# Kernel tuning notes

Hardware: AMD Instinct MI355X
Metric: run time of the kernel (lower is better)

## Reference

```python
import jax, jax.numpy as jnp
import numpy as np

T = 1024  # output_length
H = 15    # GRU hidden size
I = 10    # seed size
O = 128   # output_size
B = 512   # batch

def setup_inputs() -> dict:
    key = jax.random.key(0)
    ks = jax.random.split(key, 8)
    s = 1.0 / np.sqrt(H)
    return {
        "feed": jax.random.normal(ks[0], (B, 1, I), dtype=jnp.float32),
        "h0":   jax.random.uniform(ks[1], (B, H), dtype=jnp.float32),
        "W_ih": jax.random.normal(ks[2], (3 * H, I), dtype=jnp.float32) * s,
        "W_hh": jax.random.normal(ks[3], (3 * H, H), dtype=jnp.float32) * s,
        "b_ih": jax.random.normal(ks[4], (3 * H,), dtype=jnp.float32) * s,
        "b_hh": jax.random.normal(ks[5], (3 * H,), dtype=jnp.float32) * s,
        "W_out": jax.random.normal(ks[6], (O, H), dtype=jnp.float32) * s,
        "b_out": jnp.zeros((O,), dtype=jnp.float32),
    }

def reference(feed, h0, W_ih, W_hh, b_ih, b_hh, W_out, b_out):
    # feed is repeated along time in the original, so the input-gate
    # projection is identical at every step: compute it once.
    x = feed[:, 0, :]                         # [B, I]
    gi = x @ W_ih.T + b_ih                    # [B, 3H]
    i_r, i_z, i_n = jnp.split(gi, 3, axis=-1)  # torch GRU gate order: r, z, n

    def step(h, _):
        gh = h @ W_hh.T + b_hh                # [B, 3H]
        h_r, h_z, h_n = jnp.split(gh, 3, axis=-1)
        r = jax.nn.sigmoid(i_r + h_r)
        z = jax.nn.sigmoid(i_z + h_z)
        n = jnp.tanh(i_n + r * h_n)
        h_new = (1.0 - z) * n + z * h
        return h_new, h_new

    _, hs = jax.lax.scan(step, h0, None, length=T)  # [T, B, H]
    # Linear + sigmoid; original returns output.transpose(0,1) -> [T, B, O],
    # which scan's time-major layout already gives us.
    out = jax.nn.sigmoid(jnp.einsum("tbh,oh->tbo", hs, W_out) + b_out)
    return out
```

## Files before the change

kernel.cpp:

```cpp
#include <hip/hip_runtime.h>
#include <cstdint>

#define Tt 1024
#define Hh 15
#define Ii 10
#define Oo 128
#define Bb 512

typedef float v4f __attribute__((ext_vector_type(4)));

__device__ __forceinline__ float sigmoidf_(float x) {
    return 1.0f / (1.0f + __expf(-x));
}
__device__ __forceinline__ float tanhf_(float x) {
    return 1.0f - 2.0f / (__expf(2.0f * x) + 1.0f);
}

#define ROT(x, j) __int_as_float(__builtin_amdgcn_update_dpp( \
    0, __float_as_int(x), 0x120 + (j), 0xF, 0xF, true))

__global__ __launch_bounds__(64, 1) void gru_recur(
    const float* __restrict__ feed, const float* __restrict__ h0,
    const float* __restrict__ W_ih, const float* __restrict__ W_hh,
    const float* __restrict__ b_ih, const float* __restrict__ b_hh,
    float* __restrict__ hs)
{
    const int lane = threadIdx.x;
    const int g = lane >> 4;
    const int u = lane & 15;
    const int uu = (u < Hh) ? u : 0;
    const int b = blockIdx.x * 4 + g;

    int pr = __builtin_amdgcn_update_dpp(0, lane & 15, 0x121, 0xF, 0xF, true);
    int p0 = __builtin_amdgcn_readfirstlane(pr);
    const int dir = (p0 == 1) ? 1 : 15;

    float Wr[16], Wz[16], Wn[16];
    #pragma unroll
    for (int j = 0; j < 16; ++j) {
        int k = (uu + dir * j) & 15;
        bool ok = (k < Hh);
        int kk = ok ? k : 0;
        Wr[j] = ok ? W_hh[(uu         ) * Hh + kk] : 0.0f;
        Wz[j] = ok ? W_hh[(uu +     Hh) * Hh + kk] : 0.0f;
        Wn[j] = ok ? W_hh[(uu + 2 * Hh) * Hh + kk] : 0.0f;
    }

    float cr = b_ih[uu]          + b_hh[uu];
    float cz = b_ih[uu + Hh]     + b_hh[uu + Hh];
    float cn = b_ih[uu + 2 * Hh];
    float bn = b_hh[uu + 2 * Hh];
    #pragma unroll
    for (int i = 0; i < Ii; ++i) {
        float x = feed[b * Ii + i];
        cr += x * W_ih[(uu         ) * Ii + i];
        cz += x * W_ih[(uu +     Hh) * Ii + i];
        cn += x * W_ih[(uu + 2 * Hh) * Ii + i];
    }

    float hcur = (u < Hh) ? h0[b * Hh + uu] : 0.0f;
    size_t off = (size_t)b * 16 + u;

    for (int t = 0; t < Tt; ++t) {
        float hr[16];
        hr[0]  = hcur;
        hr[1]  = ROT(hcur, 1);   hr[2]  = ROT(hcur, 2);
        hr[3]  = ROT(hcur, 3);   hr[4]  = ROT(hcur, 4);
        hr[5]  = ROT(hcur, 5);   hr[6]  = ROT(hcur, 6);
        hr[7]  = ROT(hcur, 7);   hr[8]  = ROT(hcur, 8);
        hr[9]  = ROT(hcur, 9);   hr[10] = ROT(hcur, 10);
        hr[11] = ROT(hcur, 11);  hr[12] = ROT(hcur, 12);
        hr[13] = ROT(hcur, 13);  hr[14] = ROT(hcur, 14);
        hr[15] = ROT(hcur, 15);

        float ar[4] = {cr, 0.f, 0.f, 0.f};
        float az[4] = {cz, 0.f, 0.f, 0.f};
        float an[4] = {bn, 0.f, 0.f, 0.f};
        #pragma unroll
        for (int j = 0; j < 16; ++j) {
            ar[j & 3] += Wr[j] * hr[j];
            az[j & 3] += Wz[j] * hr[j];
            an[j & 3] += Wn[j] * hr[j];
        }
        float r = sigmoidf_((ar[0] + ar[1]) + (ar[2] + ar[3]));
        float z = sigmoidf_((az[0] + az[1]) + (az[2] + az[3]));
        float dn = (an[0] + an[1]) + (an[2] + an[3]);
        float n = tanhf_(cn + r * dn);
        float hnew = n + z * (hcur - n);

        hs[off] = hnew;
        off += (size_t)Bb * 16;
        hcur = hnew;
    }
}

__device__ __forceinline__ v4f ntload4(const float* p) {
    return __builtin_nontemporal_load((const v4f*)p);
}

__global__ __launch_bounds__(256) void gru_proj(
    const float* __restrict__ hs, const float* __restrict__ W_out,
    const float* __restrict__ b_out, float* __restrict__ out)
{
    const int q  = threadIdx.x & 31;
    const int gg = threadIdx.x >> 5;
    const int o0 = q * 4;

    float w[4][Hh];
    float bo[4];
    #pragma unroll
    for (int j = 0; j < 4; ++j) {
        bo[j] = b_out[o0 + j];
        #pragma unroll
        for (int k = 0; k < Hh; ++k) w[j][k] = W_out[(o0 + j) * Hh + k];
    }

    const int P = Tt * Bb;
    const int stride = gridDim.x * 8;
    int p = blockIdx.x * 8 + gg;
    if (p >= P) return;

    const float* hp = hs + (size_t)p * 16;
    v4f A = ntload4(hp), B_ = ntload4(hp + 4), C = ntload4(hp + 8), D = ntload4(hp + 12);

    while (true) {
        int pn = p + stride;
        bool more = pn < P;
        const float* hpn = hs + (size_t)(more ? pn : p) * 16;
        v4f A2 = ntload4(hpn), B2 = ntload4(hpn + 4),
            C2 = ntload4(hpn + 8), D2 = ntload4(hpn + 12);

        float h[Hh] = {A.x, A.y, A.z, A.w, B_.x, B_.y, B_.z, B_.w,
                       C.x, C.y, C.z, C.w, D.x, D.y, D.z};
        float acc[4];
        #pragma unroll
        for (int j = 0; j < 4; ++j) {
            float s0 = bo[j], s1 = 0.f;
            #pragma unroll
            for (int k = 0; k < Hh; k += 2) s0 += h[k] * w[j][k];
            #pragma unroll
            for (int k = 1; k < Hh; k += 2) s1 += h[k] * w[j][k];
            acc[j] = sigmoidf_(s0 + s1);
        }
        v4f res = {acc[0], acc[1], acc[2], acc[3]};
        __builtin_nontemporal_store(res, (v4f*)(out + (size_t)p * (size_t)Oo + o0));

        if (!more) break;
        p = pn; A = A2; B_ = B2; C = C2; D = D2;
    }
}

extern "C" void kernel_launch(void* const* d_in, const int* in_sizes, int n_in,
                              void* d_out, int out_size, void* d_ws, size_t ws_size,
                              hipStream_t stream) {
    const float* feed  = (const float*)d_in[0];
    const float* h0    = (const float*)d_in[1];
    const float* W_ih  = (const float*)d_in[2];
    const float* W_hh  = (const float*)d_in[3];
    const float* b_ih  = (const float*)d_in[4];
    const float* b_hh  = (const float*)d_in[5];
    const float* W_out = (const float*)d_in[6];
    const float* b_out = (const float*)d_in[7];
    float* out = (float*)d_out;
    float* hs  = (float*)d_ws;

    gru_recur<<<Bb / 4, 64, 0, stream>>>(feed, h0, W_ih, W_hh, b_ih, b_hh, hs);
    gru_proj<<<2048, 256, 0, stream>>>(hs, W_out, b_out, out);
}
```

Baseline: 528.2 us.

## Fuse GRU recurrence and output projection into one per-batch kernel

Merges the recurrence and output projection into a single kernel with one wavefront per batch element. Each step broadcasts the hidden state with readlane and each lane computes two of the 128 outputs, storing them directly. This removes the hs workspace round trip and the second launch. In exchange, the 4x redundant recurrence lanes (16 lanes each replicated), 15 serial readlanes per step and projection work now sit on the sequential critical path, and the grid grows from 128 to 512 wavefronts.

```diff
diff --git a/kernel.cpp b/kernel.cpp
--- a/kernel.cpp
+++ b/kernel.cpp
@@ -7,7 +7,7 @@
 #define Oo 128
 #define Bb 512
 
-typedef float v4f __attribute__((ext_vector_type(4)));
+typedef float v2f __attribute__((ext_vector_type(2)));
 
 __device__ __forceinline__ float sigmoidf_(float x) {
     return 1.0f / (1.0f + __expf(-x));
@@ -19,21 +19,20 @@
 #define ROT(x, j) __int_as_float(__builtin_amdgcn_update_dpp( \
     0, __float_as_int(x), 0x120 + (j), 0xF, 0xF, true))
 
-__global__ __launch_bounds__(64, 1) void gru_recur(
+__global__ __launch_bounds__(64, 1) void gru_fused(
     const float* __restrict__ feed, const float* __restrict__ h0,
     const float* __restrict__ W_ih, const float* __restrict__ W_hh,
     const float* __restrict__ b_ih, const float* __restrict__ b_hh,
-    float* __restrict__ hs)
+    const float* __restrict__ W_out, const float* __restrict__ b_out,
+    float* __restrict__ out)
 {
     const int lane = threadIdx.x;
-    const int g = lane >> 4;
     const int u = lane & 15;
     const int uu = (u < Hh) ? u : 0;
-    const int b = blockIdx.x * 4 + g;
+    const int b = blockIdx.x;
 
     int pr = __builtin_amdgcn_update_dpp(0, lane & 15, 0x121, 0xF, 0xF, true);
-    int p0 = __builtin_amdgcn_readfirstlane(pr);
-    const int dir = (p0 == 1) ? 1 : 15;
+    const int dir = (__builtin_amdgcn_readfirstlane(pr) == 1) ? 1 : 15;
 
     float Wr[16], Wz[16], Wn[16];
     #pragma unroll
@@ -58,8 +57,17 @@
         cn += x * W_ih[(uu + 2 * Hh) * Ii + i];
     }
 
+    const int o0 = lane * 2;
+    float wp0[Hh], wp1[Hh];
+    #pragma unroll
+    for (int k = 0; k < Hh; ++k) {
+        wp0[k] = W_out[(o0    ) * Hh + k];
+        wp1[k] = W_out[(o0 + 1) * Hh + k];
+    }
+    const float bo0 = b_out[o0], bo1 = b_out[o0 + 1];
+
     float hcur = (u < Hh) ? h0[b * Hh + uu] : 0.0f;
-    size_t off = (size_t)b * 16 + u;
+    float* outp = out + (size_t)b * Oo + o0;
 
     for (int t = 0; t < Tt; ++t) {
         float hr[16];
@@ -88,65 +96,28 @@
         float n = tanhf_(cn + r * dn);
         float hnew = n + z * (hcur - n);
 
-        hs[off] = hnew;
-        off += (size_t)Bb * 16;
+        float hv[Hh];
+        #pragma unroll
+        for (int k = 0; k < Hh; ++k)
+            hv[k] = __int_as_float(
+                __builtin_amdgcn_readlane(__float_as_int(hnew), k));
+
+        float s0a = bo0, s0b = 0.f, s1a = bo1, s1b = 0.f;
+        #pragma unroll
+        for (int k = 0; k < Hh; k += 2) {
+            s0a += hv[k] * wp0[k];
+            s1a += hv[k] * wp1[k];
+        }
+        #pragma unroll
+        for (int k = 1; k < Hh; k += 2) {
+            s0b += hv[k] * wp0[k];
+            s1b += hv[k] * wp1[k];
+        }
+        v2f res = {sigmoidf_(s0a + s0b), sigmoidf_(s1a + s1b)};
+        __builtin_nontemporal_store(res, (v2f*)outp);
+        outp += (size_t)Bb * Oo;
+
         hcur = hnew;
-    }
-}
-
-__device__ __forceinline__ v4f ntload4(const float* p) {
-    return __builtin_nontemporal_load((const v4f*)p);
-}
-
-__global__ __launch_bounds__(256) void gru_proj(
-    const float* __restrict__ hs, const float* __restrict__ W_out,
-    const float* __restrict__ b_out, float* __restrict__ out)
-{
-    const int q  = threadIdx.x & 31;
-    const int gg = threadIdx.x >> 5;
-    const int o0 = q * 4;
-
-    float w[4][Hh];
-    float bo[4];
-    #pragma unroll
-    for (int j = 0; j < 4; ++j) {
-        bo[j] = b_out[o0 + j];
-        #pragma unroll
-        for (int k = 0; k < Hh; ++k) w[j][k] = W_out[(o0 + j) * Hh + k];
-    }
-
-    const int P = Tt * Bb;
-    const int stride = gridDim.x * 8;
-    int p = blockIdx.x * 8 + gg;
-    if (p >= P) return;
-
-    const float* hp = hs + (size_t)p * 16;
-    v4f A = ntload4(hp), B_ = ntload4(hp + 4), C = ntload4(hp + 8), D = ntload4(hp + 12);
-
-    while (true) {
-        int pn = p + stride;
-        bool more = pn < P;
-        const float* hpn = hs + (size_t)(more ? pn : p) * 16;
-        v4f A2 = ntload4(hpn), B2 = ntload4(hpn + 4),
-            C2 = ntload4(hpn + 8), D2 = ntload4(hpn + 12);
-
-        float h[Hh] = {A.x, A.y, A.z, A.w, B_.x, B_.y, B_.z, B_.w,
-                       C.x, C.y, C.z, C.w, D.x, D.y, D.z};
-        float acc[4];
-        #pragma unroll
-        for (int j = 0; j < 4; ++j) {
-            float s0 = bo[j], s1 = 0.f;
-            #pragma unroll
-            for (int k = 0; k < Hh; k += 2) s0 += h[k] * w[j][k];
-            #pragma unroll
-            for (int k = 1; k < Hh; k += 2) s1 += h[k] * w[j][k];
-            acc[j] = sigmoidf_(s0 + s1);
-        }
-        v4f res = {acc[0], acc[1], acc[2], acc[3]};
-        __builtin_nontemporal_store(res, (v4f*)(out + (size_t)p * (size_t)Oo + o0));
-
-        if (!more) break;
-        p = pn; A = A2; B_ = B2; C = C2; D = D2;
     }
 }
 
@@ -162,8 +133,7 @@
     const float* W_out = (const float*)d_in[6];
     const float* b_out = (const float*)d_in[7];
     float* out = (float*)d_out;
-    float* hs  = (float*)d_ws;
 
-    gru_recur<<<Bb / 4, 64, 0, stream>>>(feed, h0, W_ih, W_hh, b_ih, b_hh, hs);
-    gru_proj<<<2048, 256, 0, stream>>>(hs, W_out, b_out, out);
+    gru_fused<<<Bb, 64, 0, stream>>>(feed, h0, W_ih, W_hh, b_ih, b_hh,
+                                     W_out, b_out, out);
 }
```

Result: slower. 595.9 us (+12.8%).
